# Performance work log

Measured on AMD Instinct MI355X. Metric: run time of the kernel, lower is better.

## Reference

```python
import jax, jax.numpy as jnp
import numpy as np
from math import factorial

AGG_NORM = 10.0

def _cg(l1, m1, l2, m2, l3, m3):
    if m3 != m1 + m2:
        return 0.0
    f = factorial
    pre = ((2*l3+1) * f(l3+l1-l2) * f(l3-l1+l2) * f(l1+l2-l3) / f(l1+l2+l3+1)) ** 0.5
    pre *= (f(l3+m3)*f(l3-m3)*f(l1-m1)*f(l1+m1)*f(l2-m2)*f(l2+m2)) ** 0.5
    s = 0.0
    for k in range(0, l1+l2-l3+1):
        d = [k, l1+l2-l3-k, l1-m1-k, l2+m2-k, l3-l2+m1+k, l3-l1-m2+k]
        if min(d) < 0:
            continue
        s += (-1.0)**k / np.prod([float(f(x)) for x in d])
    return pre * s

def _U(l):
    U = np.zeros((2*l+1, 2*l+1), dtype=complex)
    U[l, l] = 1.0
    s2 = 2 ** -0.5
    for m in range(1, l+1):
        U[l+m, l+m] = (-1)**m * s2
        U[l+m, l-m] = s2
        U[l-m, l-m] = 1j * s2
        U[l-m, l+m] = -1j * (-1)**m * s2
    return U

def _real_w3j(l1, l2, l3):
    w = np.zeros((2*l1+1, 2*l2+1, 2*l3+1))
    for m1 in range(-l1, l1+1):
        for m2 in range(-l2, l2+1):
            m3 = -(m1+m2)
            if abs(m3) <= l3:
                w[m1+l1, m2+l2, m3+l3] = (-1.0)**(l1-l2-m3) * _cg(l1, m1, l2, m2, l3, -m3) / (2*l3+1) ** 0.5
    R = np.einsum('im,jn,ko,mno->ijk', _U(l1), _U(l2), _U(l3), w.astype(complex))
    R = R.real if np.abs(R.real).max() >= np.abs(R.imag).max() else R.imag
    return jnp.asarray((R / np.linalg.norm(R)).astype(np.float32))

_TRIPLES = [(0,0,0),(0,1,1),(0,2,2),(1,0,1),(1,1,0),(1,1,2),(1,2,1),(2,0,2),(2,1,1),(2,2,0),(2,2,2),(2,2,4)]
W3J = {t: _real_w3j(*t) for t in _TRIPLES}
PATHS1 = [(0,0,0),(0,1,1),(0,2,2)]
PATHS2 = [(0,0,0),(0,1,1),(0,2,2),(1,0,1),(1,1,0),(1,1,2),(1,2,1),(2,0,2),(2,1,1),(2,2,0),(2,2,2)]
PATHS_P = [(0,0,0),(0,2,2),(2,0,2),(2,2,0),(2,2,2)]
PATHS_4 = [(0,0,0),(2,2,0),(0,2,2),(2,0,2),(2,2,2),(2,2,4)]

def _cart_basis():
    # 21-dim orthonormal basis of rank-4 tensors with ijkl=ijlk=jikl=klij symmetry
    pairs = [(0,0),(1,1),(2,2),(1,2),(0,2),(0,1)]
    mats = []
    for i, j in pairs:
        A = np.zeros((3,3)); A[i,j] = 1.0; A[j,i] = 1.0
        mats.append(A / np.linalg.norm(A))
    B = []
    for a in range(6):
        for b in range(a, 6):
            T = 0.5*(np.einsum('ij,kl->ijkl', mats[a], mats[b]) + np.einsum('ij,kl->ijkl', mats[b], mats[a]))
            B.append(T / np.linalg.norm(T))
    return jnp.asarray(np.stack(B).astype(np.float32))
B21 = _cart_basis()
_MI = np.array([0,1,2,1,0,0]); _MJ = np.array([0,1,2,2,2,1])
_MF = jnp.asarray(np.array([1,1,1,2**0.5,2**0.5,2**0.5], dtype=np.float32))

def _sh(u):
    # component-normalized real spherical harmonics, l=0..2
    x, y, z = u[:,0], u[:,1], u[:,2]
    s0 = jnp.ones_like(x)[:, None]
    s1 = 3**0.5 * u
    s2 = jnp.stack([15**0.5*x*y, 15**0.5*y*z, 5**0.5/2*(3*z*z-1), 15**0.5*x*z, 15**0.5/2*(x*x-y*y)], axis=1)
    return [s0, s1, s2]

def _gauss(x, start, end, n):
    v = jnp.linspace(start, end, n)
    step = (end - start) / (n - 1)
    return jnp.exp(-(((x[:, None] - v) / step) ** 2)) / 1.12

def _lin(x, w):
    return jnp.einsum('nck,cd->ndk', x, w)

def _interaction(xs, sh, ef, senders, receivers, n_nodes, up_w, m1, m2, lin_w, lin_b, paths, norm):
    ups = [None if x is None else _lin(x, up_w[i]) for i, x in enumerate(xs)]
    E = ef.shape[0]
    w = (jax.nn.silu(ef @ m1) @ m2).reshape(E, len(paths), -1)
    gath = {l: ups[l][senders] for l in range(len(ups)) if ups[l] is not None}
    msgs = {}
    for p, (l1, l2, l3) in enumerate(paths):
        m = jnp.einsum('eci,ej,ijk,ec->eck', gath[l1], sh[l2], W3J[(l1, l2, l3)], w[:, p, :])
        msgs[l3] = msgs[l3] + m if l3 in msgs else m
    out = []
    for l in (0, 1, 2):
        agg = jax.ops.segment_sum(msgs[l], receivers, num_segments=n_nodes) / norm
        y = _lin(agg, lin_w[l])
        if l == 0:
            y = y + lin_b[None, :, None]
        out.append(y)
    return out

def _ctp(a, b, pw):
    out = {}
    for p, (l1, l2, l3) in enumerate(PATHS_P):
        m = jnp.einsum('gci,gcj,ijk,c->gck', a[l1], b[l2], W3J[(l1, l2, l3)], pw[p])
        out[l3] = out[l3] + m if l3 in out else m
    return out

def _forward(positions, node_attrs, edge_attr, shifts, W_embed, b_embed, up1_w, mlp1_w1, mlp1_w2, lin1_w, lin1_b, up2_w, mlp2_w1, mlp2_w2, lin2_w, lin2_b, ro_lin_w, ro_gate_w, ro_gate_b, ro_lin2_w, glin_w0, glin_b0, glin_w2, prod_pw2, prod_pw3, prod_lin, fo_w, edge_index, batch, num_graphs):
    N = positions.shape[0]
    senders, receivers = edge_index[0], edge_index[1]
    x0 = (node_attrs @ W_embed + b_embed)[:, :, None]            # [N,64,1]
    vec = positions[receivers] - positions[senders] + shifts
    length = jnp.linalg.norm(vec, axis=1, keepdims=True)
    sh = _sh(vec / (length + 1e-9))
    ef = jnp.concatenate([_gauss(length[:, 0], 0.0, 0.6, 6), _gauss(edge_attr[:, 0], 0.0, 0.03, 6)], axis=1)
    xs = _interaction([x0], sh, ef, senders, receivers, N, up1_w, mlp1_w1, mlp1_w2, lin1_w, lin1_b, PATHS1, AGG_NORM)
    xs = _interaction(xs, sh, ef, senders, receivers, N, up2_w, mlp2_w1, mlp2_w2, lin2_w, lin2_b, PATHS2, AGG_NORM)
    h = [_lin(xs[l], ro_lin_w[l]) for l in range(3)]
    gates = jax.nn.silu(xs[0][:, :, 0] @ ro_gate_w + ro_gate_b)  # [N,128]
    y0 = jax.nn.silu(h[0]); y1 = h[1] * gates[:, :64, None]; y2 = h[2] * gates[:, 64:, None]
    y = [_lin(a, ro_lin2_w[i]) for i, a in enumerate((y0, y1, y2))]
    cnt = jnp.clip(jax.ops.segment_sum(jnp.ones((N,), y[0].dtype), batch, num_segments=num_graphs), 1.0)
    g = [jax.ops.segment_sum(a, batch, num_segments=num_graphs) / cnt[:, None, None] for a in y]
    r = {0: _lin(g[0], glin_w0) + glin_b0[None, :, None], 2: _lin(g[2], glin_w2)}
    t2 = _ctp(r, r, prod_pw2)
    t3 = _ctp(t2, r, prod_pw3)
    r = {l: _lin(r[l], prod_lin[0, i]) + _lin(t2[l], prod_lin[1, i]) + _lin(t3[l], prod_lin[2, i]) for i, l in enumerate((0, 2))}
    outs = {}
    for p, (l1, l2, l3) in enumerate(PATHS_4):
        wp = fo_w[p][:, :, :1] if l3 == 4 else fo_w[p]
        m = jnp.einsum('gui,gvj,ijk,uvw->gwk', r[l1], r[l2], W3J[(l1, l2, l3)], wp)
        outs[l3] = outs[l3] + m if l3 in outs else m
    G = outs[0].shape[0]
    v = jnp.concatenate([outs[0].reshape(G, 2), outs[2].reshape(G, 10), outs[4].reshape(G, 9)], axis=1)
    stiff = jnp.einsum('ga,aijkl->gijkl', v, B21)
    C = stiff[:, _MI[:, None], _MJ[:, None], _MI[None, :], _MJ[None, :]] * (_MF[:, None] * _MF[None, :])
    return C @ C  # matrix_func = 'square'

def setup_inputs():
    k = jax.random.split(jax.random.key(0), 32)
    N, E, G, C = 20000, 200000, 128, 64
    s = lambda i, shape, sc=1.0: jax.random.normal(k[i], shape, dtype=jnp.float32) * sc
    return {
        'positions': jax.random.uniform(k[0], (N, 3), dtype=jnp.float32),
        'node_attrs': jax.random.uniform(k[1], (N, 1), dtype=jnp.float32),
        'edge_attr': jax.random.uniform(k[2], (E, 1), dtype=jnp.float32) * 0.03,
        'shifts': jnp.zeros((E, 3), jnp.float32),
        'W_embed': s(5, (1, C)),
        'b_embed': jnp.zeros((C,), jnp.float32),
        'up1_w': s(6, (1, C, C), C**-0.5),
        'mlp1_w1': s(7, (12, C), 12**-0.5),
        'mlp1_w2': s(8, (C, 3 * C), C**-0.5),
        'lin1_w': s(9, (3, C, C), C**-0.5),
        'lin1_b': jnp.zeros((C,), jnp.float32),
        'up2_w': s(10, (3, C, C), C**-0.5),
        'mlp2_w1': s(11, (12, C), 12**-0.5),
        'mlp2_w2': s(12, (C, 11 * C), C**-0.5),
        'lin2_w': s(13, (3, C, C), C**-0.5),
        'lin2_b': jnp.zeros((C,), jnp.float32),
        'ro_lin_w': s(14, (3, C, C), C**-0.5),
        'ro_gate_w': s(15, (C, 2 * C), C**-0.5),
        'ro_gate_b': jnp.zeros((2 * C,), jnp.float32),
        'ro_lin2_w': s(16, (3, C, C), C**-0.5),
        'glin_w0': s(17, (C, 16), C**-0.5),
        'glin_b0': jnp.zeros((16,), jnp.float32),
        'glin_w2': s(18, (C, 16), C**-0.5),
        'prod_pw2': s(19, (5, 16), 0.5),
        'prod_pw3': s(20, (5, 16), 0.5),
        'prod_lin': s(21, (3, 2, 16, 16), 0.25),
        'fo_w': s(22, (6, 16, 16, 2), 0.25),
        'edge_index': jax.random.randint(k[3], (2, E), 0, N),
        'batch': jnp.sort(jax.random.randint(k[4], (N,), 0, G)),
        'num_graphs': G,
    }

def reference(positions, node_attrs, edge_attr, shifts, W_embed, b_embed, up1_w, mlp1_w1, mlp1_w2, lin1_w, lin1_b, up2_w, mlp2_w1, mlp2_w2, lin2_w, lin2_b, ro_lin_w, ro_gate_w, ro_gate_b, ro_lin2_w, glin_w0, glin_b0, glin_w2, prod_pw2, prod_pw3, prod_lin, fo_w, edge_index, batch, num_graphs):
    return _forward(positions, node_attrs, edge_attr, shifts, W_embed, b_embed, up1_w, mlp1_w1, mlp1_w2, lin1_w, lin1_b, up2_w, mlp2_w1, mlp2_w2, lin2_w, lin2_b, ro_lin_w, ro_gate_w, ro_gate_b, ro_lin2_w, glin_w0, glin_b0, glin_w2, prod_pw2, prod_pw3, prod_lin, fo_w, edge_index, batch, num_graphs)
```

## Files before the change

### kernel.cpp

```cpp
#include <hip/hip_runtime.h>
#include <cmath>
#include <complex>
#include <vector>
#include <cstring>

static double hfact(int n){ double r=1; for(int i=2;i<=n;i++) r*=i; return r; }

static double hcg(int l1,int m1,int l2,int m2,int l3,int m3){
  if(m3!=m1+m2) return 0.0;
  double pre = std::sqrt((2*l3+1)*hfact(l3+l1-l2)*hfact(l3-l1+l2)*hfact(l1+l2-l3)/hfact(l1+l2+l3+1));
  pre *= std::sqrt(hfact(l3+m3)*hfact(l3-m3)*hfact(l1-m1)*hfact(l1+m1)*hfact(l2-m2)*hfact(l2+m2));
  double s=0;
  for(int k=0;k<=l1+l2-l3;k++){
    int d0=k,d1=l1+l2-l3-k,d2=l1-m1-k,d3=l2+m2-k,d4=l3-l2+m1+k,d5=l3-l1-m2+k;
    if(d0<0||d1<0||d2<0||d3<0||d4<0||d5<0) continue;
    double den=hfact(d0)*hfact(d1)*hfact(d2)*hfact(d3)*hfact(d4)*hfact(d5);
    s += ((k&1)?-1.0:1.0)/den;
  }
  return pre*s;
}

static void hU(int l, std::complex<double>* U){
  int n=2*l+1;
  for(int i=0;i<n*n;i++) U[i]=std::complex<double>(0.0,0.0);
  U[l*n+l]=1.0;
  double s2=std::sqrt(0.5);
  for(int m=1;m<=l;m++){
    double sgn=(m&1)?-1.0:1.0;
    U[(l+m)*n+(l+m)] = sgn*s2;
    U[(l+m)*n+(l-m)] = s2;
    U[(l-m)*n+(l-m)] = std::complex<double>(0.0, s2);
    U[(l-m)*n+(l+m)] = std::complex<double>(0.0, -sgn*s2);
  }
}

static void real_w3j(int l1,int l2,int l3, float* out){
  int n1=2*l1+1,n2=2*l2+1,n3=2*l3+1;
  std::vector<double> w((size_t)n1*n2*n3,0.0);
  for(int m1=-l1;m1<=l1;m1++)for(int m2=-l2;m2<=l2;m2++){
    int m3=-(m1+m2);
    if(m3<-l3||m3>l3) continue;
    int e=l1-l2-m3;
    double sgn = (((e%2)+2)%2)?-1.0:1.0;
    w[((size_t)(m1+l1)*n2+(m2+l2))*n3+(m3+l3)] = sgn*hcg(l1,m1,l2,m2,l3,-m3)/std::sqrt((double)(2*l3+1));
  }
  std::vector<std::complex<double>> U1((size_t)n1*n1),U2((size_t)n2*n2),U3((size_t)n3*n3),R((size_t)n1*n2*n3,std::complex<double>(0,0));
  hU(l1,U1.data()); hU(l2,U2.data()); hU(l3,U3.data());
  for(int i=0;i<n1;i++)for(int j=0;j<n2;j++)for(int k=0;k<n3;k++){
    std::complex<double> acc(0.0,0.0);
    for(int m=0;m<n1;m++){
      std::complex<double> u1=U1[i*n1+m]; if(u1.real()==0.0&&u1.imag()==0.0) continue;
      for(int nn=0;nn<n2;nn++){
        std::complex<double> u2=U2[j*n2+nn]; if(u2.real()==0.0&&u2.imag()==0.0) continue;
        std::complex<double> u12=u1*u2;
        for(int o=0;o<n3;o++){
          double wv=w[((size_t)m*n2+nn)*n3+o];
          if(wv!=0.0) acc += u12*U3[k*n3+o]*wv;
        }
      }
    }
    R[((size_t)i*n2+j)*n3+k]=acc;
  }
  double mre=0,mim=0;
  for(size_t t=0;t<R.size();t++){ mre=std::max(mre,std::fabs(R[t].real())); mim=std::max(mim,std::fabs(R[t].imag())); }
  bool useRe = (mre>=mim);
  double nrm=0;
  for(size_t t=0;t<R.size();t++){ double v=useRe?R[t].real():R[t].imag(); nrm+=v*v; }
  nrm=std::sqrt(nrm);
  for(size_t t=0;t<R.size();t++){ double v=useRe?R[t].real():R[t].imag(); out[t]=(float)(v/nrm); }
}

struct WAll {
  float w000;
  float w011[9];
  float w022[25];
  float w101[9];
  float w110[9];
  float w112[45];
  float w121[45];
  float w202[25];
  float w211[45];
  float w220[25];
  float w222[125];
};
struct Wg { float w000; float w022[25]; float w202[25]; float w220[25]; float w222[125]; float w224[225]; };

__device__ __forceinline__ float bcast(float v, int l){
  return __int_as_float(__builtin_amdgcn_readlane(__float_as_int(v), l));
}
__device__ __forceinline__ float silu(float x){ return x/(1.f+expf(-x)); }

__global__ __launch_bounds__(256) void k_prep(
  const float* __restrict__ We, const float* __restrict__ be, const float* __restrict__ up1,
  const float* __restrict__ lin1, const float* __restrict__ lin1b, const float* __restrict__ up2,
  float* __restrict__ M123, float* __restrict__ Svec, float* __restrict__ Tvec, float* __restrict__ bias2)
{
  int idx=blockIdx.x*256+threadIdx.x;
  if(idx<12288){
    int l=idx>>12, c=(idx>>6)&63, d=idx&63;
    float a=0;
    for(int k=0;k<64;k++) a+=lin1[l*4096+c*64+k]*up2[l*4096+k*64+d];
    M123[idx]=0.1f*a;
  } else if(idx<12352){
    int d=idx-12288; float a=0;
    for(int c=0;c<64;c++) a+=We[c]*up1[c*64+d];
    Svec[d]=a;
  } else if(idx<12416){
    int d=idx-12352; float a=0;
    for(int c=0;c<64;c++) a+=be[c]*up1[c*64+d];
    Tvec[d]=a;
  } else if(idx<12480){
    int d=idx-12416; float a=0;
    for(int c=0;c<64;c++) a+=lin1b[c]*up2[c*64+d];
    bias2[d]=a;
  }
}

__global__ __launch_bounds__(256) void k_shuf(
  const float* __restrict__ w2a, const float* __restrict__ w2b,
  float* __restrict__ T1, float* __restrict__ T2)
{
  int idx=blockIdx.x*256+threadIdx.x;
  if(idx<16384){
    int p=idx&3, c=(idx>>2)&63, h=idx>>8;
    T1[idx]=(p<3)? w2a[h*192+p*64+c] : 0.f;
  } else if(idx<16384+49152){
    int q2=idx-16384;
    int h=q2/768, rem=q2%768, qq=rem>>8, rem2=rem&255, c=rem2>>2, j=rem2&3;
    int p=qq*4+j;
    T2[q2]=(p<11)? w2b[h*704+p*64+c] : 0.f;
  }
}

__global__ __launch_bounds__(256) void k_geom(
  const float* __restrict__ pos, const float* __restrict__ shifts,
  const float* __restrict__ eattr, const int* __restrict__ eidx,
  float* __restrict__ shb, float* __restrict__ efb, float* __restrict__ Tbl,
  int E, WAll W)
{
  int e=blockIdx.x*256+threadIdx.x;
  if(e>=E) return;
  int s=eidx[e], r=eidx[E+e];
  float vx=pos[r*3+0]-pos[s*3+0]+shifts[e*3+0];
  float vy=pos[r*3+1]-pos[s*3+1]+shifts[e*3+1];
  float vz=pos[r*3+2]-pos[s*3+2]+shifts[e*3+2];
  float len=sqrtf(vx*vx+vy*vy+vz*vz);
  float inv=1.f/(len+1e-9f);
  float x=vx*inv,y=vy*inv,z=vz*inv;
  const float c3=1.7320508075688772f, c15=3.872983346207417f, c5h=1.118033988749895f, c15h=1.9364916731037085f;
  float s1[3]={c3*x, c3*y, c3*z};
  float s2[5]={c15*x*y, c15*y*z, c5h*(3.f*z*z-1.f), c15*x*z, c15h*(x*x-y*y)};
  float* sp=&shb[(size_t)e*12];
  sp[0]=1.f; sp[1]=s1[0]; sp[2]=s1[1]; sp[3]=s1[2];
  sp[4]=s2[0]; sp[5]=s2[1]; sp[6]=s2[2]; sp[7]=s2[3]; sp[8]=s2[4];
  sp[9]=0.f; sp[10]=0.f; sp[11]=0.f;
  float ea=eattr[e];
  float* fp=&efb[(size_t)e*12];
  #pragma unroll
  for(int i=0;i<6;i++){ float d=(len-0.12f*(float)i)/0.12f; fp[i]=expf(-d*d)/1.12f; }
  #pragma unroll
  for(int i=0;i<6;i++){ float d=(ea-0.006f*(float)i)/0.006f; fp[6+i]=expf(-d*d)/1.12f; }
  if(Tbl){
    float* tb=&Tbl[(size_t)e*96];
    #pragma unroll
    for(int k=0;k<3;k++) tb[k]=s1[k]*W.w011[k*4];
    tb[3]=0.f;
    #pragma unroll
    for(int k=0;k<5;k++) tb[4+k]=s2[k]*W.w022[k*6];
    tb[9]=0.f; tb[10]=0.f; tb[11]=0.f;
    #pragma unroll
    for(int i=0;i<3;i++) tb[12+i]=s1[i]*W.w110[i*4];
    tb[15]=0.f;
    #pragma unroll
    for(int i=0;i<5;i++) tb[16+i]=s2[i]*W.w220[i*6];
    tb[21]=0.f; tb[22]=0.f; tb[23]=0.f;
    #pragma unroll
    for(int i=0;i<3;i++)
      #pragma unroll
      for(int k=0;k<3;k++){ float t=0;
        #pragma unroll
        for(int j=0;j<5;j++) t+=s2[j]*W.w121[(i*5+j)*3+k];
        tb[24+i*3+k]=t; }
    tb[33]=0.f; tb[34]=0.f; tb[35]=0.f;
    #pragma unroll
    for(int i=0;i<5;i++)
      #pragma unroll
      for(int k=0;k<3;k++){ float t=0;
        #pragma unroll
        for(int j=0;j<3;j++) t+=s1[j]*W.w211[(i*3+j)*3+k];
        tb[36+i*3+k]=t; }
    tb[51]=0.f;
    #pragma unroll
    for(int i=0;i<3;i++)
      #pragma unroll
      for(int k=0;k<5;k++){ float t=0;
        #pragma unroll
        for(int j=0;j<3;j++) t+=s1[j]*W.w112[(i*3+j)*5+k];
        tb[52+i*5+k]=t; }
    tb[67]=0.f;
    #pragma unroll
    for(int i=0;i<5;i++)
      #pragma unroll
      for(int k=0;k<5;k++){ float t=0;
        #pragma unroll
        for(int j=0;j<5;j++) t+=s2[j]*W.w222[(i*5+j)*5+k];
        tb[68+i*5+k]=t; }
    tb[93]=0.f; tb[94]=0.f; tb[95]=0.f;
  }
}

template<int TBL>
__global__ __launch_bounds__(256) void k_edge1(
  const float* __restrict__ na, const float* __restrict__ SV, const float* __restrict__ TV,
  const float* __restrict__ m1, const float* __restrict__ m2T,
  const float* __restrict__ sh, const float* __restrict__ Tbl, const float* __restrict__ ef,
  const int* __restrict__ eidx, float* __restrict__ agg, int E, WAll W)
{
  __shared__ __align__(16) float wl[8*256];
  __shared__ float m1s[768];
  int tid=threadIdx.x, lane=tid&63, wid=tid>>6;
  for(int i=tid;i<768;i+=256) m1s[i]=m1[i];
  float Sv=SV[lane], Tv=TV[lane];
  __syncthreads();
  int nb=(E+31)/32;
  for(int b=blockIdx.x;b<nb;b+=gridDim.x){
    int e0=b*32+wid*8;
    float hid[8]; float acc[8][3];
    #pragma unroll
    for(int e=0;e<8;e++){
      float h=0.f;
      if(e0+e<E){
        const float4* fp=(const float4*)(ef+(size_t)(e0+e)*12);
        float4 f0=fp[0], f1=fp[1], f2=fp[2];
        h = f0.x*m1s[0*64+lane]+f0.y*m1s[1*64+lane]+f0.z*m1s[2*64+lane]+f0.w*m1s[3*64+lane]
          + f1.x*m1s[4*64+lane]+f1.y*m1s[5*64+lane]+f1.z*m1s[6*64+lane]+f1.w*m1s[7*64+lane]
          + f2.x*m1s[8*64+lane]+f2.y*m1s[9*64+lane]+f2.z*m1s[10*64+lane]+f2.w*m1s[11*64+lane];
      }
      hid[e]=silu(h);
      acc[e][0]=0; acc[e][1]=0; acc[e][2]=0;
    }
    for(int ch=0;ch<8;ch++){
      __syncthreads();
      const float4* src=(const float4*)(m2T+(size_t)ch*2048);
      float4* dst4=(float4*)wl;
      dst4[tid]=src[tid];
      dst4[tid+256]=src[tid+256];
      __syncthreads();
      #pragma unroll
      for(int h8=0;h8<8;h8++){
        int h=ch*8+h8;
        float4 mv=*(const float4*)&wl[(h8*64+lane)*4];
        #pragma unroll
        for(int e=0;e<8;e++){
          float s=bcast(hid[e],h);
          acc[e][0]+=s*mv.x; acc[e][1]+=s*mv.y; acc[e][2]+=s*mv.z;
        }
      }
    }
    #pragma unroll
    for(int e=0;e<8;e++){
      int ee=e0+e;
      if(ee>=E) continue;
      int snd=eidx[ee], rcv=eidx[E+ee];
      float g0 = na[snd]*Sv + Tv;
      float* dst=&agg[(size_t)rcv*576];
      atomicAdd(&dst[lane], g0*W.w000*acc[e][0]);
      if constexpr(TBL){
        const float* tb=&Tbl[(size_t)ee*96];
        #pragma unroll
        for(int k=0;k<3;k++)
          atomicAdd(&dst[(1+k)*64+lane], g0*acc[e][1]*tb[k]);
        #pragma unroll
        for(int k=0;k<5;k++)
          atomicAdd(&dst[(4+k)*64+lane], g0*acc[e][2]*tb[4+k]);
      } else {
        const float4* shp=(const float4*)(sh+(size_t)ee*12);
        float4 h0=shp[0], h1=shp[1], h2=shp[2];
        float s1[3]={h0.y,h0.z,h0.w};
        float s2[5]={h1.x,h1.y,h1.z,h1.w,h2.x};
        #pragma unroll
        for(int k=0;k<3;k++)
          atomicAdd(&dst[(1+k)*64+lane], g0*acc[e][1]*s1[k]*W.w011[k*4]);
        #pragma unroll
        for(int k=0;k<5;k++)
          atomicAdd(&dst[(4+k)*64+lane], g0*acc[e][2]*s2[k]*W.w022[k*6]);
      }
    }
  }
}

template<int TBL>
__global__ __launch_bounds__(256) void k_edge2(
  const float* __restrict__ ups2, const float* __restrict__ m1, const float* __restrict__ m2T,
  const float* __restrict__ sh, const float* __restrict__ Tbl, const float* __restrict__ ef,
  const int* __restrict__ eidx, float* __restrict__ agg, int E, WAll W)
{
  __shared__ __align__(16) float wl[8*768];
  __shared__ float m1s[768];
  int tid=threadIdx.x, lane=tid&63, wid=tid>>6;
  for(int i=tid;i<768;i+=256) m1s[i]=m1[i];
  __syncthreads();
  int nb=(E+15)/16;
  for(int b=blockIdx.x;b<nb;b+=gridDim.x){
    int e0=b*16+wid*4;
    float hid[4]; float acc[4][11];
    #pragma unroll
    for(int e=0;e<4;e++){
      float h=0.f;
      if(e0+e<E){
        const float4* fp=(const float4*)(ef+(size_t)(e0+e)*12);
        float4 f0=fp[0], f1=fp[1], f2=fp[2];
        h = f0.x*m1s[0*64+lane]+f0.y*m1s[1*64+lane]+f0.z*m1s[2*64+lane]+f0.w*m1s[3*64+lane]
          + f1.x*m1s[4*64+lane]+f1.y*m1s[5*64+lane]+f1.z*m1s[6*64+lane]+f1.w*m1s[7*64+lane]
          + f2.x*m1s[8*64+lane]+f2.y*m1s[9*64+lane]+f2.z*m1s[10*64+lane]+f2.w*m1s[11*64+lane];
      }
      hid[e]=silu(h);
      #pragma unroll
      for(int p=0;p<11;p++) acc[e][p]=0.f;
    }
    for(int ch=0;ch<8;ch++){
      __syncthreads();
      const float4* src=(const float4*)(m2T+(size_t)ch*6144);
      float4* dst4=(float4*)wl;
      #pragma unroll
      for(int i=0;i<6;i++) dst4[tid+i*256]=src[tid+i*256];
      __syncthreads();
      #pragma unroll
      for(int h8=0;h8<8;h8++){
        int h=ch*8+h8;
        float4 q0=*(const float4*)&wl[((h8*3+0)*64+lane)*4];
        float4 q1=*(const float4*)&wl[((h8*3+1)*64+lane)*4];
        float4 q2=*(const float4*)&wl[((h8*3+2)*64+lane)*4];
        #pragma unroll
        for(int e=0;e<4;e++){
          float s=bcast(hid[e],h);
          acc[e][0]+=s*q0.x; acc[e][1]+=s*q0.y; acc[e][2]+=s*q0.z; acc[e][3]+=s*q0.w;
          acc[e][4]+=s*q1.x; acc[e][5]+=s*q1.y; acc[e][6]+=s*q1.z; acc[e][7]+=s*q1.w;
          acc[e][8]+=s*q2.x; acc[e][9]+=s*q2.y; acc[e][10]+=s*q2.z;
        }
      }
    }
    #pragma unroll
    for(int e=0;e<4;e++){
      int ee=e0+e;
      if(ee>=E) continue;
      int snd=eidx[ee], rcv=eidx[E+ee];
      const float* up=&ups2[(size_t)snd*576];
      float a0=acc[e][0],a1=acc[e][1],a2=acc[e][2],a3=acc[e][3];
      float a4=acc[e][4],a5=acc[e][5],a6=acc[e][6],a7=acc[e][7];
      float a8=acc[e][8],a9=acc[e][9],a10=acc[e][10];
      float g0=up[lane];
      float g1[3], g2[5];
      #pragma unroll
      for(int i=0;i<3;i++) g1[i]=up[(1+i)*64+lane];
      #pragma unroll
      for(int i=0;i<5;i++) g2[i]=up[(4+i)*64+lane];
      float* dst=&agg[(size_t)rcv*576];
      if constexpr(TBL){
        const float* tb=&Tbl[(size_t)ee*96];
        {
          float t110 = g1[0]*tb[12]+g1[1]*tb[13]+g1[2]*tb[14];
          float t220 = g2[0]*tb[16]+g2[1]*tb[17]+g2[2]*tb[18]+g2[3]*tb[19]+g2[4]*tb[20];
          atomicAdd(&dst[lane], W.w000*g0*a0 + a4*t110 + a9*t220);
        }
        #pragma unroll
        for(int k=0;k<3;k++){
          float t121 = g1[0]*tb[24+k]+g1[1]*tb[27+k]+g1[2]*tb[30+k];
          float t211 = g2[0]*tb[36+k]+g2[1]*tb[39+k]+g2[2]*tb[42+k]+g2[3]*tb[45+k]+g2[4]*tb[48+k];
          float mk = g0*a1*tb[k] + a3*g1[k]*W.w101[k*4] + a6*t121 + a8*t211;
          atomicAdd(&dst[(1+k)*64+lane], mk);
        }
        #pragma unroll
        for(int k=0;k<5;k++){
          float t112 = g1[0]*tb[52+k]+g1[1]*tb[57+k]+g1[2]*tb[62+k];
          float t222 = g2[0]*tb[68+k]+g2[1]*tb[73+k]+g2[2]*tb[78+k]+g2[3]*tb[83+k]+g2[4]*tb[88+k];
          float mk = g0*a2*tb[4+k] + a7*g2[k]*W.w202[k*6] + a5*t112 + a10*t222;
          atomicAdd(&dst[(4+k)*64+lane], mk);
        }
      } else {
        const float4* shp=(const float4*)(sh+(size_t)ee*12);
        float4 h0=shp[0], h1=shp[1], h2=shp[2];
        float s1[3]={h0.y,h0.z,h0.w};
        float s2[5]={h1.x,h1.y,h1.z,h1.w,h2.x};
        {
          float t110 = g1[0]*s1[0]*W.w110[0]+g1[1]*s1[1]*W.w110[4]+g1[2]*s1[2]*W.w110[8];
          float t220 = 0;
          #pragma unroll
          for(int i=0;i<5;i++) t220 += g2[i]*s2[i]*W.w220[i*6];
          atomicAdd(&dst[lane], W.w000*g0*a0 + a4*t110 + a9*t220);
        }
        #pragma unroll
        for(int k=0;k<3;k++){
          float mk = g0*a1*s1[k]*W.w011[k*4];
          mk += a3*g1[k]*W.w101[k*4];
          float t=0;
          #pragma unroll
          for(int i=0;i<3;i++){ float u=0;
            #pragma unroll
            for(int j=0;j<5;j++) u+=s2[j]*W.w121[(i*5+j)*3+k];
            t+=g1[i]*u; }
          mk += a6*t;
          t=0;
          #pragma unroll
          for(int i=0;i<5;i++){ float u=0;
            #pragma unroll
            for(int j=0;j<3;j++) u+=s1[j]*W.w211[(i*3+j)*3+k];
            t+=g2[i]*u; }
          mk += a8*t;
          atomicAdd(&dst[(1+k)*64+lane], mk);
        }
        #pragma unroll
        for(int k=0;k<5;k++){
          float mk = g0*a2*s2[k]*W.w022[k*6];
          float t=0;
          #pragma unroll
          for(int i=0;i<3;i++){ float u=0;
            #pragma unroll
            for(int j=0;j<3;j++) u+=s1[j]*W.w112[(i*3+j)*5+k];
            t+=g1[i]*u; }
          mk += a5*t;
          mk += a7*g2[k]*W.w202[k*6];
          t=0;
          #pragma unroll
          for(int i=0;i<5;i++){ float u=0;
            #pragma unroll
            for(int j=0;j<5;j++) u+=s2[j]*W.w222[(i*5+j)*5+k];
            t+=g2[i]*u; }
          mk += a10*t;
          atomicAdd(&dst[(4+k)*64+lane], mk);
        }
      }
    }
  }
}

template<int MODE>
__global__ __launch_bounds__(256) void k_node(
  const float* __restrict__ X, float* __restrict__ Y,
  const float* __restrict__ Ms, const float* __restrict__ bias,
  const float* __restrict__ gates, const int* __restrict__ batch,
  int N, float scale)
{
  int kk=blockIdx.y;
  int l=(kk==0)?0:(kk<4)?1:2;
  __shared__ float Mt[64][68];
  const float* M=Ms+l*4096;
  int tid=threadIdx.x;
  for(int idx=tid;idx<4096;idx+=256){ int c=idx>>6,d=idx&63; Mt[d][c]=M[idx]; }
  __syncthreads();
  int lane=tid&63, wid=tid>>6;
  int n0=(blockIdx.x*4+wid)*4;
  float xr[4];
  #pragma unroll
  for(int t=0;t<4;t++){ int n=n0+t; xr[t]=(n<N)?X[(size_t)n*576+kk*64+lane]:0.f; }
  float acc[4]={0,0,0,0};
  for(int cb=0;cb<64;cb+=4){
    float4 mv=*(const float4*)&Mt[lane][cb];
    #pragma unroll
    for(int t=0;t<4;t++){
      acc[t]+=bcast(xr[t],cb+0)*mv.x;
      acc[t]+=bcast(xr[t],cb+1)*mv.y;
      acc[t]+=bcast(xr[t],cb+2)*mv.z;
      acc[t]+=bcast(xr[t],cb+3)*mv.w;
    }
  }
  #pragma unroll
  for(int t=0;t<4;t++){
    int n=n0+t; if(n>=N) break;
    float v=acc[t]*scale;
    if constexpr(MODE==0||MODE==1){
      if(kk==0) v+=bias[lane];
      Y[(size_t)n*576+kk*64+lane]=v;
    } else if constexpr(MODE==2){
      if(kk==0) v=silu(v);
      else if(kk<4) v*=gates[(size_t)n*128+lane];
      else v*=gates[(size_t)n*128+64+lane];
      Y[(size_t)n*576+kk*64+lane]=v;
    } else {
      int bg=batch[n];
      atomicAdd(&Y[(size_t)bg*576+kk*64+lane], v);
    }
  }
}

__global__ __launch_bounds__(256) void k_gates(
  const float* __restrict__ xs, const float* __restrict__ gw, const float* __restrict__ gb,
  float* __restrict__ gates, int N)
{
  __shared__ float Gt[128][68];
  int tid=threadIdx.x;
  for(int idx=tid; idx<8192; idx+=256){ int c=idx>>7, t=idx&127; Gt[t][c]=gw[c*128+t]; }
  __syncthreads();
  int lane=tid&63, wid=tid>>6;
  int n0=(blockIdx.x*4+wid)*4;
  float xr[4];
  #pragma unroll
  for(int t=0;t<4;t++){ int n=n0+t; xr[t]=(n<N)?xs[(size_t)n*576+lane]:0.f; }
  float a0[4]={0,0,0,0}, a1[4]={0,0,0,0};
  for(int cb=0;cb<64;cb+=4){
    float4 m0=*(const float4*)&Gt[lane][cb];
    float4 m1=*(const float4*)&Gt[64+lane][cb];
    #pragma unroll
    for(int t=0;t<4;t++){
      float x0=bcast(xr[t],cb), x1=bcast(xr[t],cb+1), x2=bcast(xr[t],cb+2), x3=bcast(xr[t],cb+3);
      a0[t]+=x0*m0.x+x1*m0.y+x2*m0.z+x3*m0.w;
      a1[t]+=x0*m1.x+x1*m1.y+x2*m1.z+x3*m1.w;
    }
  }
  #pragma unroll
  for(int t=0;t<4;t++){
    int n=n0+t; if(n>=N) break;
    float g0=a0[t]+gb[lane], g1=a1[t]+gb[64+lane];
    gates[(size_t)n*128+lane]=silu(g0);
    gates[(size_t)n*128+64+lane]=silu(g1);
  }
}

__global__ __launch_bounds__(256) void k_cnt(const int* __restrict__ batch, float* __restrict__ cnt, int N){
  int n=blockIdx.x*256+threadIdx.x;
  if(n<N) atomicAdd(&cnt[batch[n]], 1.f);
}

__device__ void ctp_dev(const float* a0, const float* a2, const float* b0, const float* b2,
                        const float* pw, float* o0, float* o2, int c, const Wg& W)
{
  float A0=a0[c], B0=b0[c], A2[5], B2[5];
  #pragma unroll
  for(int i=0;i<5;i++){ A2[i]=a2[c*5+i]; B2[i]=b2[c*5+i]; }
  float o = pw[0*16+c]*A0*B0*W.w000;
  { float t=0;
    #pragma unroll
    for(int i=0;i<5;i++)
      #pragma unroll
      for(int j=0;j<5;j++) t+=A2[i]*B2[j]*W.w220[i*5+j];
    o += pw[3*16+c]*t; }
  o0[c]=o;
  #pragma unroll
  for(int k=0;k<5;k++){
    float t=0;
    { float s=0;
      #pragma unroll
      for(int j=0;j<5;j++) s+=B2[j]*W.w022[j*5+k];
      t+=pw[1*16+c]*A0*s; }
    { float s=0;
      #pragma unroll
      for(int i=0;i<5;i++) s+=A2[i]*W.w202[i*5+k];
      t+=pw[2*16+c]*s*B0; }
    { float s=0;
      #pragma unroll
      for(int i=0;i<5;i++)
        #pragma unroll
        for(int j=0;j<5;j++) s+=A2[i]*B2[j]*W.w222[(i*5+j)*5+k];
      t+=pw[4*16+c]*s; }
    o2[c*5+k]=t;
  }
}

__global__ __launch_bounds__(256) void k_graph(
  const float* __restrict__ gsum, const float* __restrict__ cnt,
  const float* __restrict__ glin_w0, const float* __restrict__ glin_b0, const float* __restrict__ glin_w2,
  const float* __restrict__ pw2, const float* __restrict__ pw3, const float* __restrict__ PL,
  const float* __restrict__ fo_w, float* __restrict__ out, Wg W)
{
  int g=blockIdx.x, tid=threadIdx.x;
  __shared__ float g0[64], g2[64*5];
  __shared__ float r0[16], r2[16*5];
  __shared__ float t20[16], t22[16*5];
  __shared__ float t30[16], t32[16*5];
  __shared__ float rp0[16], rp2[16*5];
  __shared__ float outs0[2], outs2[10], outs4[9];
  __shared__ float vv[21], stf[81], Cm[36];
  __shared__ float B21s[21*81];

  if(tid<21){
    const int pi[6]={0,1,2,1,0,0}, pj[6]={0,1,2,2,2,1};
    int a=0,b=0,idx=tid;
    for(a=0;a<6;a++){ int c6=6-a; if(idx<c6){ b=a+idx; break; } idx-=c6; }
    float ma[9]; float mb[9];
    for(int x=0;x<9;x++){ ma[x]=0; mb[x]=0; }
    { float v=(pi[a]==pj[a])?1.f:0.7071067811865476f; ma[pi[a]*3+pj[a]]=v; ma[pj[a]*3+pi[a]]=v; }
    { float v=(pi[b]==pj[b])?1.f:0.7071067811865476f; mb[pi[b]*3+pj[b]]=v; mb[pj[b]*3+pi[b]]=v; }
    float T[81]; float nrm=0;
    for(int x=0;x<81;x++){
      int ij=x/9, kl=x%9;
      float t=0.5f*(ma[ij]*mb[kl]+mb[ij]*ma[kl]);
      T[x]=t; nrm+=t*t;
    }
    nrm=sqrtf(nrm);
    for(int x=0;x<81;x++) B21s[tid*81+x]=T[x]/nrm;
  }

  float cinv=1.f/fmaxf(cnt[g],1.f);
  if(tid<64){
    g0[tid]=gsum[(size_t)g*576+tid]*cinv;
    for(int k=0;k<5;k++) g2[tid*5+k]=gsum[(size_t)g*576+(4+k)*64+tid]*cinv;
  }
  __syncthreads();

  if(tid<16){
    float a=0;
    for(int c=0;c<64;c++) a+=g0[c]*glin_w0[c*16+tid];
    r0[tid]=a+glin_b0[tid];
  } else if(tid<96){
    int u=(tid-16)/5, k=(tid-16)%5; float a=0;
    for(int c=0;c<64;c++) a+=g2[c*5+k]*glin_w2[c*16+u];
    r2[u*5+k]=a;
  }
  __syncthreads();

  if(tid<16) ctp_dev(r0,r2, r0,r2, pw2, t20,t22, tid, W);
  __syncthreads();
  if(tid<16) ctp_dev(t20,t22, r0,r2, pw3, t30,t32, tid, W);
  __syncthreads();

  if(tid<16){
    int d=tid; float a=0;
    for(int c=0;c<16;c++)
      a += r0[c]*PL[(0*2+0)*256+c*16+d] + t20[c]*PL[(1*2+0)*256+c*16+d] + t30[c]*PL[(2*2+0)*256+c*16+d];
    rp0[d]=a;
  } else if(tid<96){
    int q=tid-16, d=q/5, k=q%5; float a=0;
    for(int c=0;c<16;c++)
      a += r2[c*5+k]*PL[(0*2+1)*256+c*16+d] + t22[c*5+k]*PL[(1*2+1)*256+c*16+d] + t32[c*5+k]*PL[(2*2+1)*256+c*16+d];
    rp2[d*5+k]=a;
  }
  if(tid<2) outs0[tid]=0.f;
  else if(tid<12) outs2[tid-2]=0.f;
  else if(tid<21) outs4[tid-12]=0.f;
  __syncthreads();

  {
    int u=tid>>4, v=tid&15;
    float A0=rp0[u], B0=rp0[v], A2[5], B2[5];
    #pragma unroll
    for(int i=0;i<5;i++){ A2[i]=rp2[u*5+i]; B2[i]=rp2[v*5+i]; }
    float s00 = A0*B0*W.w000;
    float s220=0;
    #pragma unroll
    for(int i=0;i<5;i++)
      #pragma unroll
      for(int j=0;j<5;j++) s220+=A2[i]*B2[j]*W.w220[i*5+j];
    float s022[5], s202[5], s222[5], s224[9];
    #pragma unroll
    for(int k=0;k<5;k++){
      float s=0;
      #pragma unroll
      for(int j=0;j<5;j++) s+=B2[j]*W.w022[j*5+k];
      s022[k]=A0*s;
      float s2v=0;
      #pragma unroll
      for(int i=0;i<5;i++) s2v+=A2[i]*W.w202[i*5+k];
      s202[k]=s2v*B0;
      float s3v=0;
      #pragma unroll
      for(int i=0;i<5;i++)
        #pragma unroll
        for(int j=0;j<5;j++) s3v+=A2[i]*B2[j]*W.w222[(i*5+j)*5+k];
      s222[k]=s3v;
    }
    #pragma unroll
    for(int k=0;k<9;k++){
      float s=0;
      #pragma unroll
      for(int i=0;i<5;i++)
        #pragma unroll
        for(int j=0;j<5;j++) s+=A2[i]*B2[j]*W.w224[(i*5+j)*9+k];
      s224[k]=s;
    }
    #pragma unroll
    for(int w=0;w<2;w++){
      float f0=fo_w[((0*16+u)*16+v)*2+w], f1=fo_w[((1*16+u)*16+v)*2+w];
      float f2=fo_w[((2*16+u)*16+v)*2+w], f3=fo_w[((3*16+u)*16+v)*2+w];
      float f4=fo_w[((4*16+u)*16+v)*2+w];
      atomicAdd(&outs0[w], s00*f0 + s220*f1);
      #pragma unroll
      for(int k=0;k<5;k++)
        atomicAdd(&outs2[w*5+k], s022[k]*f2 + s202[k]*f3 + s222[k]*f4);
    }
    float f5=fo_w[((5*16+u)*16+v)*2+0];
    #pragma unroll
    for(int k=0;k<9;k++) atomicAdd(&outs4[k], s224[k]*f5);
  }
  __syncthreads();

  if(tid<2) vv[tid]=outs0[tid];
  else if(tid<12) vv[tid]=outs2[tid-2];
  else if(tid<21) vv[tid]=outs4[tid-12];
  __syncthreads();
  if(tid<81){
    float a=0;
    for(int q=0;q<21;q++) a+=vv[q]*B21s[q*81+tid];
    stf[tid]=a;
  }
  __syncthreads();
  {
    const int MI[6]={0,1,2,1,0,0}, MJ[6]={0,1,2,2,2,1};
    const float MF[6]={1.f,1.f,1.f,1.4142135623730951f,1.4142135623730951f,1.4142135623730951f};
    if(tid<36){
      int p=tid/6, q=tid%6;
      Cm[tid]=stf[MI[p]*27+MJ[p]*9+MI[q]*3+MJ[q]]*MF[p]*MF[q];
    }
  }
  __syncthreads();
  if(tid<36){
    int p=tid/6, q=tid%6; float a=0;
    for(int r=0;r<6;r++) a+=Cm[p*6+r]*Cm[r*6+q];
    out[(size_t)g*36+tid]=a;
  }
}

extern "C" void kernel_launch(void* const* d_in, const int* in_sizes, int n_in,
                              void* d_out, int out_size, void* d_ws, size_t ws_size,
                              hipStream_t stream)
{
  const float* positions=(const float*)d_in[0];
  const float* node_attrs=(const float*)d_in[1];
  const float* edge_attr=(const float*)d_in[2];
  const float* shifts=(const float*)d_in[3];
  const float* W_embed=(const float*)d_in[4];
  const float* b_embed=(const float*)d_in[5];
  const float* up1_w=(const float*)d_in[6];
  const float* mlp1_w1=(const float*)d_in[7];
  const float* mlp1_w2=(const float*)d_in[8];
  const float* lin1_w=(const float*)d_in[9];
  const float* lin1_b=(const float*)d_in[10];
  const float* up2_w=(const float*)d_in[11];
  const float* mlp2_w1=(const float*)d_in[12];
  const float* mlp2_w2=(const float*)d_in[13];
  const float* lin2_w=(const float*)d_in[14];
  const float* lin2_b=(const float*)d_in[15];
  const float* ro_lin_w=(const float*)d_in[16];
  const float* ro_gate_w=(const float*)d_in[17];
  const float* ro_gate_b=(const float*)d_in[18];
  const float* ro_lin2_w=(const float*)d_in[19];
  const float* glin_w0=(const float*)d_in[20];
  const float* glin_b0=(const float*)d_in[21];
  const float* glin_w2=(const float*)d_in[22];
  const float* prod_pw2=(const float*)d_in[23];
  const float* prod_pw3=(const float*)d_in[24];
  const float* prod_lin=(const float*)d_in[25];
  const float* fo_w=(const float*)d_in[26];
  const int* edge_index=(const int*)d_in[27];
  const int* batch=(const int*)d_in[28];
  const int N=in_sizes[1];
  const int E=in_sizes[2];
  const int G=128;
  float* out=(float*)d_out;

  float* p=(float*)d_ws;
  float* shb=p;    p+=(size_t)12*E;
  float* efb=p;    p+=(size_t)12*E;
  float* bufA=p;   p+=(size_t)N*576;
  float* bufB=p;   p+=(size_t)N*576;
  float* gatesb=p; p+=(size_t)N*128;
  float* M123=p;   p+=3*4096;
  float* Svec=p;   p+=64;
  float* Tvec=p;   p+=64;
  float* bias2=p;  p+=64;
  float* m2T1=p;   p+=16384;
  float* m2T2=p;   p+=49152;
  float* gsum=p;   p+=(size_t)G*576;
  float* cntb=p;   p+=G;
  size_t baseNeed=(size_t)(p-(float*)d_ws)*sizeof(float);
  if(baseNeed>ws_size) return;
  float* Tbl=p;
  bool useTbl = (baseNeed + (size_t)96*E*sizeof(float)) <= ws_size;
  if(!useTbl) Tbl=nullptr;

  WAll wa; Wg wg;
  {
    float t000[1],t011[9],t022[25],t101[9],t110[9],t112[45],t121[45],t202[25],t211[45],t220[25],t222[125],t224[225];
    real_w3j(0,0,0,t000); real_w3j(0,1,1,t011); real_w3j(0,2,2,t022);
    real_w3j(1,0,1,t101); real_w3j(1,1,0,t110); real_w3j(1,1,2,t112); real_w3j(1,2,1,t121);
    real_w3j(2,0,2,t202); real_w3j(2,1,1,t211); real_w3j(2,2,0,t220); real_w3j(2,2,2,t222); real_w3j(2,2,4,t224);
    wa.w000=t000[0];
    std::memcpy(wa.w011,t011,sizeof t011); std::memcpy(wa.w022,t022,sizeof t022);
    std::memcpy(wa.w101,t101,sizeof t101); std::memcpy(wa.w110,t110,sizeof t110);
    std::memcpy(wa.w112,t112,sizeof t112); std::memcpy(wa.w121,t121,sizeof t121);
    std::memcpy(wa.w202,t202,sizeof t202); std::memcpy(wa.w211,t211,sizeof t211);
    std::memcpy(wa.w220,t220,sizeof t220); std::memcpy(wa.w222,t222,sizeof t222);
    wg.w000=t000[0];
    std::memcpy(wg.w022,t022,sizeof t022); std::memcpy(wg.w202,t202,sizeof t202);
    std::memcpy(wg.w220,t220,sizeof t220); std::memcpy(wg.w222,t222,sizeof t222);
    std::memcpy(wg.w224,t224,sizeof t224);
  }

  k_prep<<<49,256,0,stream>>>(W_embed,b_embed,up1_w,lin1_w,lin1_b,up2_w,M123,Svec,Tvec,bias2);
  k_shuf<<<256,256,0,stream>>>(mlp1_w2,mlp2_w2,m2T1,m2T2);
  k_geom<<<(E+255)/256,256,0,stream>>>(positions,shifts,edge_attr,edge_index,shb,efb,Tbl,E,wa);

  hipMemsetAsync(bufA,0,(size_t)N*576*sizeof(float),stream);
  const int eblocks=1280;
  if(useTbl)
    k_edge1<1><<<eblocks,256,0,stream>>>(node_attrs,Svec,Tvec,mlp1_w1,m2T1,shb,Tbl,efb,edge_index,bufA,E,wa);
  else
    k_edge1<0><<<eblocks,256,0,stream>>>(node_attrs,Svec,Tvec,mlp1_w1,m2T1,shb,Tbl,efb,edge_index,bufA,E,wa);

  dim3 ngrid((N+15)/16,9);
  k_node<0><<<ngrid,256,0,stream>>>(bufA,bufB,M123,bias2,nullptr,nullptr,N,1.0f);

  hipMemsetAsync(bufA,0,(size_t)N*576*sizeof(float),stream);
  if(useTbl)
    k_edge2<1><<<eblocks,256,0,stream>>>(bufB,mlp2_w1,m2T2,shb,Tbl,efb,edge_index,bufA,E,wa);
  else
    k_edge2<0><<<eblocks,256,0,stream>>>(bufB,mlp2_w1,m2T2,shb,Tbl,efb,edge_index,bufA,E,wa);

  k_node<1><<<ngrid,256,0,stream>>>(bufA,bufB,lin2_w,lin2_b,nullptr,nullptr,N,0.1f);
  k_gates<<<(N+15)/16,256,0,stream>>>(bufB,ro_gate_w,ro_gate_b,gatesb,N);
  k_node<2><<<ngrid,256,0,stream>>>(bufB,bufA,ro_lin_w,nullptr,gatesb,nullptr,N,1.0f);

  hipMemsetAsync(gsum,0,((size_t)G*576+G)*sizeof(float),stream);
  k_cnt<<<(N+255)/256,256,0,stream>>>(batch,cntb,N);
  k_node<3><<<ngrid,256,0,stream>>>(bufA,gsum,ro_lin2_w,nullptr,nullptr,batch,N,1.0f);

  k_graph<<<G,256,0,stream>>>(gsum,cntb,glin_w0,glin_b0,glin_w2,prod_pw2,prod_pw3,prod_lin,fo_w,out,wg);
}
```

Before: 1.476 ms.

## Sort edges by receiver and coalesce per-receiver atomics in edge kernels

Adds a counting sort of edges by receiver, made of a histogram, a single-block scan and a scatter. Geometry outputs are written in the sorted order, and both edge kernels read the sorted sender and receiver arrays. Each wave now sums contributions for consecutive edges that share a receiver in registers before issuing atomics, which cuts global atomic traffic. The cost is several extra small kernels, including a serial single-block scan over N, and the scatter order is nondeterministic, so summation order can vary between runs.

Result: faster. 1.349 ms, median of 2 (-8.6%).

```diff
diff --git a/kernel.cpp b/kernel.cpp
--- a/kernel.cpp
+++ b/kernel.cpp
@@ -132,15 +132,59 @@
   }
 }
 
+__global__ __launch_bounds__(256) void k_hist(const int* __restrict__ eidx, int* __restrict__ hist, int E){
+  int e=blockIdx.x*256+threadIdx.x;
+  if(e<E) atomicAdd(&hist[eidx[E+e]], 1);
+}
+
+__global__ __launch_bounds__(256) void k_scan(const int* __restrict__ hist, int* __restrict__ offs, int N){
+  __shared__ int tmp[256];
+  __shared__ int carry;
+  int tid=threadIdx.x;
+  if(tid==0) carry=0;
+  __syncthreads();
+  for(int base=0;base<N;base+=256){
+    int v=(base+tid<N)? hist[base+tid]:0;
+    tmp[tid]=v;
+    __syncthreads();
+    for(int off=1;off<256;off<<=1){
+      int add=(tid>=off)? tmp[tid-off]:0;
+      __syncthreads();
+      tmp[tid]+=add;
+      __syncthreads();
+    }
+    if(base+tid<N) offs[base+tid]=tmp[tid]-v+carry;
+    __syncthreads();
+    if(tid==0) carry+=tmp[255];
+    __syncthreads();
+  }
+}
+
+__global__ __launch_bounds__(256) void k_scatter(
+  const int* __restrict__ eidx, int* __restrict__ offs,
+  int* __restrict__ posOf, int* __restrict__ sndS, int* __restrict__ rcvS, int E)
+{
+  int e=blockIdx.x*256+threadIdx.x;
+  if(e<E){
+    int r=eidx[E+e];
+    int pos=atomicAdd(&offs[r],1);
+    posOf[e]=pos;
+    sndS[pos]=eidx[e];
+    rcvS[pos]=r;
+  }
+}
+
 __global__ __launch_bounds__(256) void k_geom(
   const float* __restrict__ pos, const float* __restrict__ shifts,
   const float* __restrict__ eattr, const int* __restrict__ eidx,
+  const int* __restrict__ posOf,
   float* __restrict__ shb, float* __restrict__ efb, float* __restrict__ Tbl,
   int E, WAll W)
 {
   int e=blockIdx.x*256+threadIdx.x;
   if(e>=E) return;
   int s=eidx[e], r=eidx[E+e];
+  int ps=posOf[e];
   float vx=pos[r*3+0]-pos[s*3+0]+shifts[e*3+0];
   float vy=pos[r*3+1]-pos[s*3+1]+shifts[e*3+1];
   float vz=pos[r*3+2]-pos[s*3+2]+shifts[e*3+2];
@@ -150,18 +194,18 @@
   const float c3=1.7320508075688772f, c15=3.872983346207417f, c5h=1.118033988749895f, c15h=1.9364916731037085f;
   float s1[3]={c3*x, c3*y, c3*z};
   float s2[5]={c15*x*y, c15*y*z, c5h*(3.f*z*z-1.f), c15*x*z, c15h*(x*x-y*y)};
-  float* sp=&shb[(size_t)e*12];
+  float* sp=&shb[(size_t)ps*12];
   sp[0]=1.f; sp[1]=s1[0]; sp[2]=s1[1]; sp[3]=s1[2];
   sp[4]=s2[0]; sp[5]=s2[1]; sp[6]=s2[2]; sp[7]=s2[3]; sp[8]=s2[4];
   sp[9]=0.f; sp[10]=0.f; sp[11]=0.f;
   float ea=eattr[e];
-  float* fp=&efb[(size_t)e*12];
+  float* fp=&efb[(size_t)ps*12];
   #pragma unroll
   for(int i=0;i<6;i++){ float d=(len-0.12f*(float)i)/0.12f; fp[i]=expf(-d*d)/1.12f; }
   #pragma unroll
   for(int i=0;i<6;i++){ float d=(ea-0.006f*(float)i)/0.006f; fp[6+i]=expf(-d*d)/1.12f; }
   if(Tbl){
-    float* tb=&Tbl[(size_t)e*96];
+    float* tb=&Tbl[(size_t)ps*96];
     #pragma unroll
     for(int k=0;k<3;k++) tb[k]=s1[k]*W.w011[k*4];
     tb[3]=0.f;
@@ -214,7 +258,8 @@
   const float* __restrict__ na, const float* __restrict__ SV, const float* __restrict__ TV,
   const float* __restrict__ m1, const float* __restrict__ m2T,
   const float* __restrict__ sh, const float* __restrict__ Tbl, const float* __restrict__ ef,
-  const int* __restrict__ eidx, float* __restrict__ agg, int E, WAll W)
+  const int* __restrict__ sndS, const int* __restrict__ rcvS,
+  float* __restrict__ agg, int E, WAll W)
 {
   __shared__ __align__(16) float wl[8*256];
   __shared__ float m1s[768];
@@ -257,34 +302,53 @@
         }
       }
     }
+    float carry[9];
+    #pragma unroll
+    for(int k=0;k<9;k++) carry[k]=0.f;
+    int lastR=-1;
     #pragma unroll
     for(int e=0;e<8;e++){
       int ee=e0+e;
-      if(ee>=E) continue;
-      int snd=eidx[ee], rcv=eidx[E+ee];
+      if(ee>=E) break;
+      int snd=sndS[ee], rcv=rcvS[ee];
+      if(lastR>=0 && rcv!=lastR){
+        float* dst=&agg[(size_t)lastR*576];
+        atomicAdd(&dst[lane], carry[0]);
+        #pragma unroll
+        for(int k=0;k<3;k++) atomicAdd(&dst[(1+k)*64+lane], carry[1+k]);
+        #pragma unroll
+        for(int k=0;k<5;k++) atomicAdd(&dst[(4+k)*64+lane], carry[4+k]);
+        #pragma unroll
+        for(int k=0;k<9;k++) carry[k]=0.f;
+      }
       float g0 = na[snd]*Sv + Tv;
-      float* dst=&agg[(size_t)rcv*576];
-      atomicAdd(&dst[lane], g0*W.w000*acc[e][0]);
       if constexpr(TBL){
         const float* tb=&Tbl[(size_t)ee*96];
-        #pragma unroll
-        for(int k=0;k<3;k++)
-          atomicAdd(&dst[(1+k)*64+lane], g0*acc[e][1]*tb[k]);
-        #pragma unroll
-        for(int k=0;k<5;k++)
-          atomicAdd(&dst[(4+k)*64+lane], g0*acc[e][2]*tb[4+k]);
+        carry[0]+=g0*W.w000*acc[e][0];
+        #pragma unroll
+        for(int k=0;k<3;k++) carry[1+k]+=g0*acc[e][1]*tb[k];
+        #pragma unroll
+        for(int k=0;k<5;k++) carry[4+k]+=g0*acc[e][2]*tb[4+k];
       } else {
         const float4* shp=(const float4*)(sh+(size_t)ee*12);
         float4 h0=shp[0], h1=shp[1], h2=shp[2];
         float s1[3]={h0.y,h0.z,h0.w};
         float s2[5]={h1.x,h1.y,h1.z,h1.w,h2.x};
-        #pragma unroll
-        for(int k=0;k<3;k++)
-          atomicAdd(&dst[(1+k)*64+lane], g0*acc[e][1]*s1[k]*W.w011[k*4]);
-        #pragma unroll
-        for(int k=0;k<5;k++)
-          atomicAdd(&dst[(4+k)*64+lane], g0*acc[e][2]*s2[k]*W.w022[k*6]);
+        carry[0]+=g0*W.w000*acc[e][0];
+        #pragma unroll
+        for(int k=0;k<3;k++) carry[1+k]+=g0*acc[e][1]*s1[k]*W.w011[k*4];
+        #pragma unroll
+        for(int k=0;k<5;k++) carry[4+k]+=g0*acc[e][2]*s2[k]*W.w022[k*6];
       }
+      lastR=rcv;
+    }
+    if(lastR>=0){
+      float* dst=&agg[(size_t)lastR*576];
+      atomicAdd(&dst[lane], carry[0]);
+      #pragma unroll
+      for(int k=0;k<3;k++) atomicAdd(&dst[(1+k)*64+lane], carry[1+k]);
+      #pragma unroll
+      for(int k=0;k<5;k++) atomicAdd(&dst[(4+k)*64+lane], carry[4+k]);
     }
   }
 }
@@ -293,7 +357,8 @@
 __global__ __launch_bounds__(256) void k_edge2(
   const float* __restrict__ ups2, const float* __restrict__ m1, const float* __restrict__ m2T,
   const float* __restrict__ sh, const float* __restrict__ Tbl, const float* __restrict__ ef,
-  const int* __restrict__ eidx, float* __restrict__ agg, int E, WAll W)
+  const int* __restrict__ sndS, const int* __restrict__ rcvS,
+  float* __restrict__ agg, int E, WAll W)
 {
   __shared__ __align__(16) float wl[8*768];
   __shared__ float m1s[768];
@@ -340,11 +405,25 @@
         }
       }
     }
+    float carry[9];
+    #pragma unroll
+    for(int k=0;k<9;k++) carry[k]=0.f;
+    int lastR=-1;
     #pragma unroll
     for(int e=0;e<4;e++){
       int ee=e0+e;
-      if(ee>=E) continue;
-      int snd=eidx[ee], rcv=eidx[E+ee];
+      if(ee>=E) break;
+      int snd=sndS[ee], rcv=rcvS[ee];
+      if(lastR>=0 && rcv!=lastR){
+        float* dst=&agg[(size_t)lastR*576];
+        atomicAdd(&dst[lane], carry[0]);
+        #pragma unroll
+        for(int k=0;k<3;k++) atomicAdd(&dst[(1+k)*64+lane], carry[1+k]);
+        #pragma unroll
+        for(int k=0;k<5;k++) atomicAdd(&dst[(4+k)*64+lane], carry[4+k]);
+        #pragma unroll
+        for(int k=0;k<9;k++) carry[k]=0.f;
+      }
       const float* up=&ups2[(size_t)snd*576];
       float a0=acc[e][0],a1=acc[e][1],a2=acc[e][2],a3=acc[e][3];
       float a4=acc[e][4],a5=acc[e][5],a6=acc[e][6],a7=acc[e][7];
@@ -355,27 +434,24 @@
       for(int i=0;i<3;i++) g1[i]=up[(1+i)*64+lane];
       #pragma unroll
       for(int i=0;i<5;i++) g2[i]=up[(4+i)*64+lane];
-      float* dst=&agg[(size_t)rcv*576];
       if constexpr(TBL){
         const float* tb=&Tbl[(size_t)ee*96];
         {
           float t110 = g1[0]*tb[12]+g1[1]*tb[13]+g1[2]*tb[14];
           float t220 = g2[0]*tb[16]+g2[1]*tb[17]+g2[2]*tb[18]+g2[3]*tb[19]+g2[4]*tb[20];
-          atomicAdd(&dst[lane], W.w000*g0*a0 + a4*t110 + a9*t220);
+          carry[0] += W.w000*g0*a0 + a4*t110 + a9*t220;
         }
         #pragma unroll
         for(int k=0;k<3;k++){
           float t121 = g1[0]*tb[24+k]+g1[1]*tb[27+k]+g1[2]*tb[30+k];
           float t211 = g2[0]*tb[36+k]+g2[1]*tb[39+k]+g2[2]*tb[42+k]+g2[3]*tb[45+k]+g2[4]*tb[48+k];
-          float mk = g0*a1*tb[k] + a3*g1[k]*W.w101[k*4] + a6*t121 + a8*t211;
-          atomicAdd(&dst[(1+k)*64+lane], mk);
+          carry[1+k] += g0*a1*tb[k] + a3*g1[k]*W.w101[k*4] + a6*t121 + a8*t211;
         }
         #pragma unroll
         for(int k=0;k<5;k++){
           float t112 = g1[0]*tb[52+k]+g1[1]*tb[57+k]+g1[2]*tb[62+k];
           float t222 = g2[0]*tb[68+k]+g2[1]*tb[73+k]+g2[2]*tb[78+k]+g2[3]*tb[83+k]+g2[4]*tb[88+k];
-          float mk = g0*a2*tb[4+k] + a7*g2[k]*W.w202[k*6] + a5*t112 + a10*t222;
-          atomicAdd(&dst[(4+k)*64+lane], mk);
+          carry[4+k] += g0*a2*tb[4+k] + a7*g2[k]*W.w202[k*6] + a5*t112 + a10*t222;
         }
       } else {
         const float4* shp=(const float4*)(sh+(size_t)ee*12);
@@ -387,7 +463,7 @@
           float t220 = 0;
           #pragma unroll
           for(int i=0;i<5;i++) t220 += g2[i]*s2[i]*W.w220[i*6];
-          atomicAdd(&dst[lane], W.w000*g0*a0 + a4*t110 + a9*t220);
+          carry[0] += W.w000*g0*a0 + a4*t110 + a9*t220;
         }
         #pragma unroll
         for(int k=0;k<3;k++){
@@ -407,7 +483,7 @@
             for(int j=0;j<3;j++) u+=s1[j]*W.w211[(i*3+j)*3+k];
             t+=g2[i]*u; }
           mk += a8*t;
-          atomicAdd(&dst[(1+k)*64+lane], mk);
+          carry[1+k]+=mk;
         }
         #pragma unroll
         for(int k=0;k<5;k++){
@@ -427,9 +503,18 @@
             for(int j=0;j<5;j++) u+=s2[j]*W.w222[(i*5+j)*5+k];
             t+=g2[i]*u; }
           mk += a10*t;
-          atomicAdd(&dst[(4+k)*64+lane], mk);
+          carry[4+k]+=mk;
         }
       }
+      lastR=rcv;
+    }
+    if(lastR>=0){
+      float* dst=&agg[(size_t)lastR*576];
+      atomicAdd(&dst[lane], carry[0]);
+      #pragma unroll
+      for(int k=0;k<3;k++) atomicAdd(&dst[(1+k)*64+lane], carry[1+k]);
+      #pragma unroll
+      for(int k=0;k<5;k++) atomicAdd(&dst[(4+k)*64+lane], carry[4+k]);
     }
   }
 }
@@ -761,6 +846,10 @@
   float* m2T2=p;   p+=49152;
   float* gsum=p;   p+=(size_t)G*576;
   float* cntb=p;   p+=G;
+  int* offs=(int*)p;   p+=N;
+  int* posOf=(int*)p;  p+=E;
+  int* sndS=(int*)p;   p+=E;
+  int* rcvS=(int*)p;   p+=E;
   size_t baseNeed=(size_t)(p-(float*)d_ws)*sizeof(float);
   if(baseNeed>ws_size) return;
   float* Tbl=p;
@@ -787,23 +876,30 @@
 
   k_prep<<<49,256,0,stream>>>(W_embed,b_embed,up1_w,lin1_w,lin1_b,up2_w,M123,Svec,Tvec,bias2);
   k_shuf<<<256,256,0,stream>>>(mlp1_w2,mlp2_w2,m2T1,m2T2);
-  k_geom<<<(E+255)/256,256,0,stream>>>(positions,shifts,edge_attr,edge_index,shb,efb,Tbl,E,wa);
+
+  hipMemsetAsync(offs,0,(size_t)N*sizeof(int),stream);
+  k_hist<<<(E+255)/256,256,0,stream>>>(edge_index,offs,E);
+  k_scan<<<1,256,0,stream>>>(offs,posOf,N);
+  hipMemcpyAsync(offs,posOf,(size_t)N*sizeof(int),hipMemcpyDeviceToDevice,stream);
+  k_scatter<<<(E+255)/256,256,0,stream>>>(edge_index,offs,posOf,sndS,rcvS,E);
+
+  k_geom<<<(E+255)/256,256,0,stream>>>(positions,shifts,edge_attr,edge_index,posOf,shb,efb,Tbl,E,wa);
 
   hipMemsetAsync(bufA,0,(size_t)N*576*sizeof(float),stream);
   const int eblocks=1280;
   if(useTbl)
-    k_edge1<1><<<eblocks,256,0,stream>>>(node_attrs,Svec,Tvec,mlp1_w1,m2T1,shb,Tbl,efb,edge_index,bufA,E,wa);
+    k_edge1<1><<<eblocks,256,0,stream>>>(node_attrs,Svec,Tvec,mlp1_w1,m2T1,shb,Tbl,efb,sndS,rcvS,bufA,E,wa);
   else
-    k_edge1<0><<<eblocks,256,0,stream>>>(node_attrs,Svec,Tvec,mlp1_w1,m2T1,shb,Tbl,efb,edge_index,bufA,E,wa);
+    k_edge1<0><<<eblocks,256,0,stream>>>(node_attrs,Svec,Tvec,mlp1_w1,m2T1,shb,Tbl,efb,sndS,rcvS,bufA,E,wa);
 
   dim3 ngrid((N+15)/16,9);
   k_node<0><<<ngrid,256,0,stream>>>(bufA,bufB,M123,bias2,nullptr,nullptr,N,1.0f);
 
   hipMemsetAsync(bufA,0,(size_t)N*576*sizeof(float),stream);
   if(useTbl)
-    k_edge2<1><<<eblocks,256,0,stream>>>(bufB,mlp2_w1,m2T2,shb,Tbl,efb,edge_index,bufA,E,wa);
+    k_edge2<1><<<eblocks,256,0,stream>>>(bufB,mlp2_w1,m2T2,shb,Tbl,efb,sndS,rcvS,bufA,E,wa);
   else
-    k_edge2<0><<<eblocks,256,0,stream>>>(bufB,mlp2_w1,m2T2,shb,Tbl,efb,edge_index,bufA,E,wa);
+    k_edge2<0><<<eblocks,256,0,stream>>>(bufB,mlp2_w1,m2T2,shb,Tbl,efb,sndS,rcvS,bufA,E,wa);
 
   k_node<1><<<ngrid,256,0,stream>>>(bufA,bufB,lin2_w,lin2_b,nullptr,nullptr,N,0.1f);
   k_gates<<<(N+15)/16,256,0,stream>>>(bufB,ro_gate_w,ro_gate_b,gatesb,N);
```
